# Performance work log

Hardware: AMD Instinct MI355X
Metric: run time of the kernel (lower is better)

Reference implementation:

```python
import jax, jax.numpy as jnp
import numpy as np
from jax.ops import segment_sum

N_NODES = 50000
N_EDGES = 800000
D_IN = 128
D_HID = 128
D_OUT = 128
N_GRAPHS = 512


def setup_inputs() -> dict:
    key = jax.random.key(0)
    ks = jax.random.split(key, 10)
    x = jax.random.normal(ks[0], (N_NODES, D_IN), dtype=jnp.float32)
    edge_index = jax.random.randint(ks[1], (2, N_EDGES), 0, N_NODES, dtype=jnp.int64)
    batch = jnp.sort(jax.random.randint(ks[2], (N_NODES,), 0, N_GRAPHS, dtype=jnp.int64))
    def glorot(k, fan_in, fan_out):
        lim = (6.0 / (fan_in + fan_out)) ** 0.5
        return jax.random.uniform(k, (fan_in, fan_out), jnp.float32, -lim, lim)
    W1 = glorot(ks[3], D_IN, D_HID)
    b1 = jnp.zeros((D_HID,), jnp.float32)
    W2 = glorot(ks[4], D_HID, D_HID)
    b2 = jnp.zeros((D_HID,), jnp.float32)
    W3 = glorot(ks[5], D_HID, D_OUT)
    b3 = jnp.zeros((D_OUT,), jnp.float32)
    return {"x": x, "edge_index": edge_index, "batch": batch,
            "W1": W1, "b1": b1, "W2": W2, "b2": b2, "W3": W3, "b3": b3}


def _gcn_conv(x, src, dst, norm, W, b, n_nodes):
    # PyG GCNConv: out[i] = sum_{j->i} norm_ji * (x_j @ W) + b
    h = x @ W                                   # [N, d_out]
    msg = norm[:, None] * h[src]                # [E+N, d_out] gathered messages
    out = segment_sum(msg, dst, num_segments=n_nodes)
    return out + b


def reference(x, edge_index, batch, W1, b1, W2, b2, W3, b3):
    n = x.shape[0]
    # add self-loops (GCNConv default)
    loop = jnp.arange(n, dtype=edge_index.dtype)
    src = jnp.concatenate([edge_index[0], loop])
    dst = jnp.concatenate([edge_index[1], loop])
    # symmetric normalization: deg counted at target with self-loops
    deg = segment_sum(jnp.ones_like(dst, dtype=x.dtype), dst, num_segments=n)
    dinv = jnp.where(deg > 0, jax.lax.rsqrt(deg), 0.0)
    norm = dinv[src] * dinv[dst]                # [E+N]
    h = jax.nn.relu(_gcn_conv(x, src, dst, norm, W1, b1, n))
    h = jax.nn.relu(_gcn_conv(h, src, dst, norm, W2, b2, n))
    h = _gcn_conv(h, src, dst, norm, W3, b3, n)
    # global_add_pool over batch ids
    return segment_sum(h, batch, num_segments=N_GRAPHS)
```

## Files before the change

### kernel.cpp

```cpp
#include <hip/hip_runtime.h>
#include <cstdint>
#include <cstddef>


typedef __attribute__((ext_vector_type(8))) short short8b;
typedef __attribute__((ext_vector_type(4))) float f32x4;

static inline int cdiv_i(int a, int b) { return (a + b - 1) / b; }

__device__ inline unsigned short f2bf(float f) {
    union { float f; unsigned int u; } v; v.f = f;
    unsigned int r = v.u + 0x7fffu + ((v.u >> 16) & 1u);
    return (unsigned short)(r >> 16);
}
__device__ inline float bf2f(unsigned short b) {
    union { unsigned int u; float f; } v; v.u = ((unsigned int)b) << 16;
    return v.f;
}

__global__ void zero_i32_kernel(int* __restrict__ p, int n) {
    int i = blockIdx.x * 256 + threadIdx.x;
    if (i < n) p[i] = 0;
}
__global__ void count_kernel(const int* __restrict__ dst, int* __restrict__ cnt, int E) {
    int i = blockIdx.x * 256 + threadIdx.x;
    if (i < E) atomicAdd(&cnt[dst[i]], 1);
}
__global__ void dinv_kernel(const int* __restrict__ cnt, float* __restrict__ dinv, int n) {
    int i = blockIdx.x * 256 + threadIdx.x;
    if (i < n) dinv[i] = rsqrtf((float)(cnt[i] + 1));
}

__global__ __launch_bounds__(256) void scan_blocksum_kernel(const int* __restrict__ cnt,
                                                            int* __restrict__ psum, int n) {
    __shared__ int ws[4];
    int b = blockIdx.x, tid = threadIdx.x;
    int i0 = b * 1024 + tid * 4;
    int s = 0;
    if (i0 + 3 < n) {
        int4 v = *(const int4*)(cnt + i0);
        s = v.x + v.y + v.z + v.w;
    } else {
        for (int j = 0; j < 4; ++j) if (i0 + j < n) s += cnt[i0 + j];
    }
    #pragma unroll
    for (int d = 1; d < 64; d <<= 1) s += __shfl_xor(s, d, 64);
    int lane = tid & 63, wid = tid >> 6;
    if (lane == 0) ws[wid] = s;
    __syncthreads();
    if (tid == 0) psum[b] = ws[0] + ws[1] + ws[2] + ws[3];
}

__global__ void scan_partials_kernel(const int* __restrict__ psum, int* __restrict__ pbase,
                                     int* __restrict__ off, int n, int np) {
    int lane = threadIdx.x;
    int v = (lane < np) ? psum[lane] : 0;
    int s = v;
    #pragma unroll
    for (int d = 1; d < 64; d <<= 1) {
        int u = __shfl_up(s, d, 64);
        if (lane >= d) s += u;
    }
    if (lane < np) pbase[lane] = s - v;
    if (lane == 63) off[n] = s;
}

__global__ __launch_bounds__(256) void scan_final_kernel(const int* __restrict__ cnt,
                                                         const int* __restrict__ pbase,
                                                         int* __restrict__ off, int n) {
    __shared__ int wsum[4];
    int b = blockIdx.x, tid = threadIdx.x;
    int lane = tid & 63, wid = tid >> 6;
    int i0 = b * 1024 + tid * 4;
    int v0 = (i0 + 0 < n) ? cnt[i0 + 0] : 0;
    int v1 = (i0 + 1 < n) ? cnt[i0 + 1] : 0;
    int v2 = (i0 + 2 < n) ? cnt[i0 + 2] : 0;
    int v3 = (i0 + 3 < n) ? cnt[i0 + 3] : 0;
    int local = v0 + v1 + v2 + v3;
    int s = local;
    #pragma unroll
    for (int d = 1; d < 64; d <<= 1) {
        int u = __shfl_up(s, d, 64);
        if (lane >= d) s += u;
    }
    if (lane == 63) wsum[wid] = s;
    __syncthreads();
    int woff = 0;
    for (int w = 0; w < wid; ++w) woff += wsum[w];
    int excl = pbase[b] + woff + (s - local);
    if (i0 + 0 < n) off[i0 + 0] = excl;
    if (i0 + 1 < n) off[i0 + 1] = excl + v0;
    if (i0 + 2 < n) off[i0 + 2] = excl + v0 + v1;
    if (i0 + 3 < n) off[i0 + 3] = excl + v0 + v1 + v2;
}

__global__ void copy_i32_kernel(const int* __restrict__ a, int* __restrict__ b, int n) {
    int i = blockIdx.x * 256 + threadIdx.x;
    if (i < n) b[i] = a[i];
}

__global__ void fill_kernel(const int* __restrict__ src, const int* __restrict__ dst,
                            const float* __restrict__ dinv, int* __restrict__ cursor,
                            int* __restrict__ csr_src, float* __restrict__ csr_norm, int E) {
    int i = blockIdx.x * 256 + threadIdx.x;
    if (i < E) {
        int s = src[i], d = dst[i];
        int pos = atomicAdd(&cursor[d], 1);
        csr_src[pos] = s;
        csr_norm[pos] = dinv[s] * dinv[d];
    }
}

__global__ void split_x_kernel(const float* __restrict__ x,
                               unsigned short* __restrict__ xh,
                               unsigned short* __restrict__ xl, int n4) {
    int i = blockIdx.x * 256 + threadIdx.x;
    if (i >= n4) return;
    float4 v = ((const float4*)x)[i];
    unsigned short h0 = f2bf(v.x), h1 = f2bf(v.y), h2 = f2bf(v.z), h3 = f2bf(v.w);
    unsigned short l0 = f2bf(v.x - bf2f(h0)), l1 = f2bf(v.y - bf2f(h1));
    unsigned short l2 = f2bf(v.z - bf2f(h2)), l3 = f2bf(v.w - bf2f(h3));
    ushort4 hv; hv.x = h0; hv.y = h1; hv.z = h2; hv.w = h3;
    ushort4 lv; lv.x = l0; lv.y = l1; lv.z = l2; lv.w = l3;
    ((ushort4*)xh)[i] = hv;
    ((ushort4*)xl)[i] = lv;
}

__global__ void split_w_kernel(const float* __restrict__ W,
                               unsigned short* __restrict__ Wh,
                               unsigned short* __restrict__ Wl) {
    int t = blockIdx.x * 256 + threadIdx.x;
    if (t >= 16384) return;
    int j = t & 7, lane = (t >> 3) & 63, ct = (t >> 9) & 7, kt = (t >> 12) & 3;
    int k = kt * 32 + (lane >> 4) * 8 + j;
    int nn = ct * 16 + (lane & 15);
    float w = W[k * 128 + nn];
    unsigned short h = f2bf(w);
    Wh[t] = h;
    Wl[t] = f2bf(w - bf2f(h));
}

__global__ __launch_bounds__(256) void gemm_mfma_kernel(
    const unsigned short* __restrict__ Ahi, const unsigned short* __restrict__ Alo,
    const unsigned short* __restrict__ Whf, const unsigned short* __restrict__ Wlf,
    unsigned short* __restrict__ hout, int n) {
    int wave = threadIdx.x >> 6, lane = threadIdx.x & 63;
    int r0 = blockIdx.x * 64 + wave * 16;
    int arow = r0 + (lane & 15);
    int la = min(arow, n - 1);
    int kgrp = (lane >> 4) * 8;

    f32x4 acc[8];
    #pragma unroll
    for (int c = 0; c < 8; ++c) acc[c] = (f32x4){0.f, 0.f, 0.f, 0.f};

    #pragma unroll
    for (int kt = 0; kt < 4; ++kt) {
        int koff = kt * 32 + kgrp;
        short8b a_h = *(const short8b*)(Ahi + (size_t)la * 128 + koff);
        short8b a_l = *(const short8b*)(Alo + (size_t)la * 128 + koff);
        const unsigned short* wb = Whf + ((size_t)(kt * 8) * 64 + lane) * 8;
        const unsigned short* lb = Wlf + ((size_t)(kt * 8) * 64 + lane) * 8;
        #pragma unroll
        for (int ct = 0; ct < 8; ++ct) {
            short8b wh = *(const short8b*)(wb + (size_t)ct * 512);
            short8b wl = *(const short8b*)(lb + (size_t)ct * 512);
            acc[ct] = __builtin_amdgcn_mfma_f32_16x16x32_bf16(a_h, wh, acc[ct], 0, 0, 0);
            acc[ct] = __builtin_amdgcn_mfma_f32_16x16x32_bf16(a_l, wh, acc[ct], 0, 0, 0);
            acc[ct] = __builtin_amdgcn_mfma_f32_16x16x32_bf16(a_h, wl, acc[ct], 0, 0, 0);
        }
    }
    int rb = r0 + (lane >> 4) * 4;
    int col = lane & 15;
    #pragma unroll
    for (int ct = 0; ct < 8; ++ct)
        #pragma unroll
        for (int i = 0; i < 4; ++i) {
            int rr = rb + i;
            if (rr < n) hout[(size_t)rr * 128 + ct * 16 + col] = f2bf(acc[ct][i]);
        }
}

template <int RELU, int MODE>
__global__ __launch_bounds__(256) void agg_kernel(
    const unsigned short* __restrict__ h, const int* __restrict__ off,
    const int* __restrict__ csr_src, const float* __restrict__ csr_norm,
    const float* __restrict__ dinv, const float* __restrict__ bias,
    unsigned short* __restrict__ ah, unsigned short* __restrict__ al,
    float* __restrict__ cf32, int n) {
    int node = blockIdx.x * 4 + (threadIdx.x >> 6);
    if (node >= n) return;
    int lane = threadIdx.x & 63;
    int ep = lane >> 4;
    int cg = lane & 15;
    int c0 = cg * 8;

    float acc[8];
    #pragma unroll
    for (int j = 0; j < 8; ++j) acc[j] = 0.f;

    if (ep == 0) {
        float di = dinv[node];
        float w = di * di;
        short8b v = *(const short8b*)(h + (size_t)node * 128 + c0);
        #pragma unroll
        for (int j = 0; j < 8; ++j) acc[j] = w * bf2f((unsigned short)v[j]);
    }
    int e0 = off[node], e1 = off[node + 1];
    for (int e = e0 + ep; e < e1; e += 4) {
        int s = csr_src[e];
        float w = csr_norm[e];
        short8b v = *(const short8b*)(h + (size_t)s * 128 + c0);
        #pragma unroll
        for (int j = 0; j < 8; ++j) acc[j] = fmaf(w, bf2f((unsigned short)v[j]), acc[j]);
    }
    #pragma unroll
    for (int j = 0; j < 8; ++j) {
        acc[j] += __shfl_xor(acc[j], 16, 64);
        acc[j] += __shfl_xor(acc[j], 32, 64);
    }
    if (ep == 0) {
        float r[8];
        #pragma unroll
        for (int j = 0; j < 8; ++j) {
            r[j] = acc[j] + bias[c0 + j];
            if (RELU) r[j] = fmaxf(r[j], 0.f);
        }
        if (MODE == 1) {
            float4 lo = make_float4(r[0], r[1], r[2], r[3]);
            float4 hi = make_float4(r[4], r[5], r[6], r[7]);
            *(float4*)(cf32 + (size_t)node * 128 + c0) = lo;
            *(float4*)(cf32 + (size_t)node * 128 + c0 + 4) = hi;
        } else {
            short8b hv, lv;
            #pragma unroll
            for (int j = 0; j < 8; ++j) {
                unsigned short hb = f2bf(r[j]);
                hv[j] = (short)hb;
                lv[j] = (short)f2bf(r[j] - bf2f(hb));
            }
            *(short8b*)(ah + (size_t)node * 128 + c0) = hv;
            *(short8b*)(al + (size_t)node * 128 + c0) = lv;
        }
    }
}

__global__ __launch_bounds__(256) void pool_kernel(const float* __restrict__ hsrc,
                                                   const int* __restrict__ batch,
                                                   float* __restrict__ out, int n) {
    __shared__ int s_lo, s_hi;
    __shared__ float red[4][128];
    int g = blockIdx.x;
    if (threadIdx.x == 0) {
        int lo = 0, hi = n;
        while (lo < hi) { int m = (lo + hi) >> 1; if (batch[m] < g) lo = m + 1; else hi = m; }
        s_lo = lo;
        lo = 0; hi = n;
        while (lo < hi) { int m = (lo + hi) >> 1; if (batch[m] < g + 1) lo = m + 1; else hi = m; }
        s_hi = lo;
    }
    __syncthreads();
    int lo = s_lo, hi = s_hi;
    int wave = threadIdx.x >> 6, lane = threadIdx.x & 63;
    int c2 = lane * 2;
    float ax = 0.f, ay = 0.f;
    for (int i = lo + wave; i < hi; i += 4) {
        float2 v = *(const float2*)(hsrc + (size_t)i * 128 + c2);
        ax += v.x; ay += v.y;
    }
    red[wave][c2] = ax;
    red[wave][c2 + 1] = ay;
    __syncthreads();
    if (wave == 0) {
        float a = red[0][c2] + red[1][c2] + red[2][c2] + red[3][c2];
        float b = red[0][c2 + 1] + red[1][c2 + 1] + red[2][c2 + 1] + red[3][c2 + 1];
        *(float2*)(out + (size_t)g * 128 + c2) = make_float2(a, b);
    }
}

extern "C" void kernel_launch(void* const* d_in, const int* in_sizes, int n_in,
                              void* d_out, int out_size, void* d_ws, size_t ws_size,
                              hipStream_t stream) {
    const float* x   = (const float*)d_in[0];
    const int*   ei  = (const int*)d_in[1];
    const int*   bat = (const int*)d_in[2];
    const float* W1  = (const float*)d_in[3];
    const float* b1  = (const float*)d_in[4];
    const float* W2  = (const float*)d_in[5];
    const float* b2  = (const float*)d_in[6];
    const float* W3  = (const float*)d_in[7];
    const float* b3  = (const float*)d_in[8];
    float* outp = (float*)d_out;

    const int N = in_sizes[0] / 128;
    const int E = in_sizes[1] / 2;
    const int NG = out_size / 128;
    const int* src = ei;
    const int* dst = ei + E;
    const int NP = cdiv_i(N, 1024);

    char* p = (char*)d_ws;
    auto alloc = [&](size_t bytes) -> void* {
        void* r = (void*)p;
        p += (bytes + 255) & ~(size_t)255;
        return r;
    };
    int*   cnt      = (int*)alloc((size_t)N * 4);
    int*   off      = (int*)alloc((size_t)(N + 1) * 4);
    int*   cursor   = (int*)alloc((size_t)N * 4);
    float* dinv     = (float*)alloc((size_t)N * 4);
    int*   psum     = (int*)alloc((size_t)(NP + 1) * 4);
    int*   pbase    = (int*)alloc((size_t)(NP + 1) * 4);
    int*   csr_src  = (int*)alloc((size_t)E * 4);
    float* csr_norm = (float*)alloc((size_t)E * 4);
    unsigned short* Hb = (unsigned short*)alloc((size_t)N * 128 * 2);
    unsigned short* Ah = (unsigned short*)alloc((size_t)N * 128 * 2);
    unsigned short* Al = (unsigned short*)alloc((size_t)N * 128 * 2);
    float* Cf = (float*)alloc((size_t)N * 128 * 4);
    unsigned short* W1h = (unsigned short*)alloc(16384 * 2);
    unsigned short* W1l = (unsigned short*)alloc(16384 * 2);
    unsigned short* W2h = (unsigned short*)alloc(16384 * 2);
    unsigned short* W2l = (unsigned short*)alloc(16384 * 2);
    unsigned short* W3h = (unsigned short*)alloc(16384 * 2);
    unsigned short* W3l = (unsigned short*)alloc(16384 * 2);

    hipLaunchKernelGGL(zero_i32_kernel, dim3(cdiv_i(N, 256)), dim3(256), 0, stream, cnt, N);
    hipLaunchKernelGGL(count_kernel, dim3(cdiv_i(E, 256)), dim3(256), 0, stream, dst, cnt, E);
    hipLaunchKernelGGL(dinv_kernel, dim3(cdiv_i(N, 256)), dim3(256), 0, stream, cnt, dinv, N);
    hipLaunchKernelGGL(scan_blocksum_kernel, dim3(NP), dim3(256), 0, stream, cnt, psum, N);
    hipLaunchKernelGGL(scan_partials_kernel, dim3(1), dim3(64), 0, stream,
                       psum, pbase, off, N, NP);
    hipLaunchKernelGGL(scan_final_kernel, dim3(NP), dim3(256), 0, stream, cnt, pbase, off, N);
    hipLaunchKernelGGL(copy_i32_kernel, dim3(cdiv_i(N, 256)), dim3(256), 0, stream, off, cursor, N);
    hipLaunchKernelGGL(fill_kernel, dim3(cdiv_i(E, 256)), dim3(256), 0, stream,
                       src, dst, dinv, cursor, csr_src, csr_norm, E);
    hipLaunchKernelGGL(split_x_kernel, dim3(cdiv_i(N * 32, 256)), dim3(256), 0, stream,
                       x, Ah, Al, N * 32);
    hipLaunchKernelGGL(split_w_kernel, dim3(64), dim3(256), 0, stream, W1, W1h, W1l);
    hipLaunchKernelGGL(split_w_kernel, dim3(64), dim3(256), 0, stream, W2, W2h, W2l);
    hipLaunchKernelGGL(split_w_kernel, dim3(64), dim3(256), 0, stream, W3, W3h, W3l);

    const int gemm_grid = cdiv_i(N, 64);
    const int agg_grid  = cdiv_i(N, 4);

    hipLaunchKernelGGL(gemm_mfma_kernel, dim3(gemm_grid), dim3(256), 0, stream,
                       Ah, Al, W1h, W1l, Hb, N);
    hipLaunchKernelGGL((agg_kernel<1, 0>), dim3(agg_grid), dim3(256), 0, stream,
                       Hb, off, csr_src, csr_norm, dinv, b1, Ah, Al, Cf, N);
    hipLaunchKernelGGL(gemm_mfma_kernel, dim3(gemm_grid), dim3(256), 0, stream,
                       Ah, Al, W2h, W2l, Hb, N);
    hipLaunchKernelGGL((agg_kernel<1, 0>), dim3(agg_grid), dim3(256), 0, stream,
                       Hb, off, csr_src, csr_norm, dinv, b2, Ah, Al, Cf, N);
    hipLaunchKernelGGL(gemm_mfma_kernel, dim3(gemm_grid), dim3(256), 0, stream,
                       Ah, Al, W3h, W3l, Hb, N);
    hipLaunchKernelGGL((agg_kernel<0, 1>), dim3(agg_grid), dim3(256), 0, stream,
                       Hb, off, csr_src, csr_norm, dinv, b3, Ah, Al, Cf, N);
    hipLaunchKernelGGL(pool_kernel, dim3(NG), dim3(256), 0, stream, Cf, bat, outp, N);
}
```

Baseline: 365.6 us.

## Factor GCN symmetric normalization into GEMM epilogue and aggregation finalization

The per-edge norm dinv[s]*dinv[d] is factored out. The source-side dinv is applied to each row in the GEMM epilogue, and the destination-side dinv is applied once per node after aggregation. This removes the csr_norm array, its build in fill_kernel, the per-edge norm loads in all three aggregation passes, and the FMA multiply per element. Scaling by dinv before the bf16 rounding changes the numerics slightly.

After: 376.3 us. 1.03x slower.

```diff
diff --git a/kernel.cpp b/kernel.cpp
--- a/kernel.cpp
+++ b/kernel.cpp
@@ -100,14 +100,12 @@
 }
 
 __global__ void fill_kernel(const int* __restrict__ src, const int* __restrict__ dst,
-                            const float* __restrict__ dinv, int* __restrict__ cursor,
-                            int* __restrict__ csr_src, float* __restrict__ csr_norm, int E) {
+                            int* __restrict__ cursor, int* __restrict__ csr_src, int E) {
     int i = blockIdx.x * 256 + threadIdx.x;
     if (i < E) {
         int s = src[i], d = dst[i];
         int pos = atomicAdd(&cursor[d], 1);
         csr_src[pos] = s;
-        csr_norm[pos] = dinv[s] * dinv[d];
     }
 }
 
@@ -143,6 +141,7 @@
 __global__ __launch_bounds__(256) void gemm_mfma_kernel(
     const unsigned short* __restrict__ Ahi, const unsigned short* __restrict__ Alo,
     const unsigned short* __restrict__ Whf, const unsigned short* __restrict__ Wlf,
+    const float* __restrict__ dinv,
     unsigned short* __restrict__ hout, int n) {
     int wave = threadIdx.x >> 6, lane = threadIdx.x & 63;
     int r0 = blockIdx.x * 64 + wave * 16;
@@ -172,19 +171,22 @@
     }
     int rb = r0 + (lane >> 4) * 4;
     int col = lane & 15;
+    float dv[4];
+    #pragma unroll
+    for (int i = 0; i < 4; ++i) dv[i] = dinv[min(rb + i, n - 1)];
     #pragma unroll
     for (int ct = 0; ct < 8; ++ct)
         #pragma unroll
         for (int i = 0; i < 4; ++i) {
             int rr = rb + i;
-            if (rr < n) hout[(size_t)rr * 128 + ct * 16 + col] = f2bf(acc[ct][i]);
+            if (rr < n) hout[(size_t)rr * 128 + ct * 16 + col] = f2bf(acc[ct][i] * dv[i]);
         }
 }
 
 template <int RELU, int MODE>
 __global__ __launch_bounds__(256) void agg_kernel(
     const unsigned short* __restrict__ h, const int* __restrict__ off,
-    const int* __restrict__ csr_src, const float* __restrict__ csr_norm,
+    const int* __restrict__ csr_src,
     const float* __restrict__ dinv, const float* __restrict__ bias,
     unsigned short* __restrict__ ah, unsigned short* __restrict__ al,
     float* __restrict__ cf32, int n) {
@@ -200,19 +202,16 @@
     for (int j = 0; j < 8; ++j) acc[j] = 0.f;
 
     if (ep == 0) {
-        float di = dinv[node];
-        float w = di * di;
         short8b v = *(const short8b*)(h + (size_t)node * 128 + c0);
         #pragma unroll
-        for (int j = 0; j < 8; ++j) acc[j] = w * bf2f((unsigned short)v[j]);
+        for (int j = 0; j < 8; ++j) acc[j] = bf2f((unsigned short)v[j]);
     }
     int e0 = off[node], e1 = off[node + 1];
     for (int e = e0 + ep; e < e1; e += 4) {
         int s = csr_src[e];
-        float w = csr_norm[e];
         short8b v = *(const short8b*)(h + (size_t)s * 128 + c0);
         #pragma unroll
-        for (int j = 0; j < 8; ++j) acc[j] = fmaf(w, bf2f((unsigned short)v[j]), acc[j]);
+        for (int j = 0; j < 8; ++j) acc[j] += bf2f((unsigned short)v[j]);
     }
     #pragma unroll
     for (int j = 0; j < 8; ++j) {
@@ -220,10 +219,11 @@
         acc[j] += __shfl_xor(acc[j], 32, 64);
     }
     if (ep == 0) {
+        float dn = dinv[node];
         float r[8];
         #pragma unroll
         for (int j = 0; j < 8; ++j) {
-            r[j] = acc[j] + bias[c0 + j];
+            r[j] = fmaf(dn, acc[j], bias[c0 + j]);
             if (RELU) r[j] = fmaxf(r[j], 0.f);
         }
         if (MODE == 1) {
@@ -312,7 +312,6 @@
     int*   psum     = (int*)alloc((size_t)(NP + 1) * 4);
     int*   pbase    = (int*)alloc((size_t)(NP + 1) * 4);
     int*   csr_src  = (int*)alloc((size_t)E * 4);
-    float* csr_norm = (float*)alloc((size_t)E * 4);
     unsigned short* Hb = (unsigned short*)alloc((size_t)N * 128 * 2);
     unsigned short* Ah = (unsigned short*)alloc((size_t)N * 128 * 2);
     unsigned short* Al = (unsigned short*)alloc((size_t)N * 128 * 2);
@@ -333,7 +332,7 @@
     hipLaunchKernelGGL(scan_final_kernel, dim3(NP), dim3(256), 0, stream, cnt, pbase, off, N);
     hipLaunchKernelGGL(copy_i32_kernel, dim3(cdiv_i(N, 256)), dim3(256), 0, stream, off, cursor, N);
     hipLaunchKernelGGL(fill_kernel, dim3(cdiv_i(E, 256)), dim3(256), 0, stream,
-                       src, dst, dinv, cursor, csr_src, csr_norm, E);
+                       src, dst, cursor, csr_src, E);
     hipLaunchKernelGGL(split_x_kernel, dim3(cdiv_i(N * 32, 256)), dim3(256), 0, stream,
                        x, Ah, Al, N * 32);
     hipLaunchKernelGGL(split_w_kernel, dim3(64), dim3(256), 0, stream, W1, W1h, W1l);
@@ -344,16 +343,16 @@
     const int agg_grid  = cdiv_i(N, 4);
 
     hipLaunchKernelGGL(gemm_mfma_kernel, dim3(gemm_grid), dim3(256), 0, stream,
-                       Ah, Al, W1h, W1l, Hb, N);
+                       Ah, Al, W1h, W1l, dinv, Hb, N);
     hipLaunchKernelGGL((agg_kernel<1, 0>), dim3(agg_grid), dim3(256), 0, stream,
-                       Hb, off, csr_src, csr_norm, dinv, b1, Ah, Al, Cf, N);
+                       Hb, off, csr_src, dinv, b1, Ah, Al, Cf, N);
     hipLaunchKernelGGL(gemm_mfma_kernel, dim3(gemm_grid), dim3(256), 0, stream,
-                       Ah, Al, W2h, W2l, Hb, N);
+                       Ah, Al, W2h, W2l, dinv, Hb, N);
     hipLaunchKernelGGL((agg_kernel<1, 0>), dim3(agg_grid), dim3(256), 0, stream,
-                       Hb, off, csr_src, csr_norm, dinv, b2, Ah, Al, Cf, N);
+                       Hb, off, csr_src, dinv, b2, Ah, Al, Cf, N);
     hipLaunchKernelGGL(gemm_mfma_kernel, dim3(gemm_grid), dim3(256), 0, stream,
-                       Ah, Al, W3h, W3l, Hb, N);
+                       Ah, Al, W3h, W3l, dinv, Hb, N);
     hipLaunchKernelGGL((agg_kernel<0, 1>), dim3(agg_grid), dim3(256), 0, stream,
-                       Hb, off, csr_src, csr_norm, dinv, b3, Ah, Al, Cf, N);
+                       Hb, off, csr_src, dinv, b3, Ah, Al, Cf, N);
     hipLaunchKernelGGL(pool_kernel, dim3(NG), dim3(256), 0, stream, Cf, bat, outp, N);
 }
```
